# Kernel tuning notes

Hardware: AMD Instinct MI355X
Metric: run time of the kernel (lower is better)

The kernel has to match this reference:

```python
import jax, jax.numpy as jnp
import numpy as np

EPS = 1e-5
GROUPS = 32


def _groupnorm(x, gamma, beta):
    B, C, H, W = x.shape
    xr = x.reshape(B, GROUPS, C // GROUPS, H, W)
    mu = xr.mean(axis=(2, 3, 4), keepdims=True)
    var = xr.var(axis=(2, 3, 4), keepdims=True)
    xn = ((xr - mu) * jax.lax.rsqrt(var + EPS)).reshape(B, C, H, W)
    return xn * gamma[None, :, None, None] + beta[None, :, None, None]


def _conv1x1(x, w, b):
    # x: [B,C,H,W], w: [Cout,Cin], b: [Cout]
    return jnp.einsum('bchw,oc->bohw', x, w) + b[None, :, None, None]


def setup_inputs() -> dict:
    key = jax.random.key(0)
    ks = jax.random.split(key, 11)
    B, C, H, W = 4, 64, 64, 64
    s = 0.05  # weight scale for well-conditioned softmax
    inp = {
        'x': jax.random.normal(ks[0], (B, C, H, W), jnp.float32),
        'gn_gamma': jnp.ones((C,), jnp.float32),
        'gn_beta': jnp.zeros((C,), jnp.float32),
        'wq': jax.random.normal(ks[1], (C, C), jnp.float32) * s,
        'bq': jnp.zeros((C,), jnp.float32),
        'wk': jax.random.normal(ks[2], (C, C), jnp.float32) * s,
        'bk': jnp.zeros((C,), jnp.float32),
        'wv': jax.random.normal(ks[3], (C, C), jnp.float32) * s,
        'bv': jnp.zeros((C,), jnp.float32),
        'wp': jax.random.normal(ks[4], (C, C), jnp.float32) * s,
        'bp': jnp.zeros((C,), jnp.float32),
    }
    return inp


def reference(x, gn_gamma, gn_beta, wq, bq, wk, bk, wv, bv, wp, bp):
    B, C, H, W = x.shape
    h = _groupnorm(x, gn_gamma, gn_beta)
    q = _conv1x1(h, wq, bq)
    k = _conv1x1(h, wk, bk)
    v = _conv1x1(h, wv, bv)
    # scores over all spatial positions: [B,H,W,H,W]
    scale = 1.0 / jnp.sqrt(jnp.asarray(C, x.dtype))
    w = jnp.einsum('bchw,bcHW->bhwHW', q, k) * scale
    w = jax.nn.softmax(w.reshape(B, H, W, H * W), axis=-1).reshape(B, H, W, H, W)
    h = jnp.einsum('bhwHW,bcHW->bchw', w, v)
    h = _conv1x1(h, wp, bp)
    return x + h
```

## Files before the change

kernel.cpp:

```cpp
#include <hip/hip_runtime.h>
#include <stdint.h>

#define Bn 4
#define Cn 64
#define Sn 4096
#define Gn 32

typedef float v4f __attribute__((ext_vector_type(4)));
typedef short v8s __attribute__((ext_vector_type(8)));
typedef short v4s __attribute__((ext_vector_type(4)));

#define MFMA16(a,b,c) __builtin_amdgcn_mfma_f32_16x16x32_bf16((a),(b),(c),0,0,0)

__device__ __forceinline__ float bf2f(uint16_t u){
  union { uint32_t i; float f; } x; x.i = ((uint32_t)u) << 16; return x.f;
}
__device__ __forceinline__ uint16_t f2bf(float f){
  union { float f; uint32_t i; } x; x.f = f;
  uint32_t r = x.i + 0x7fffu + ((x.i >> 16) & 1u);
  return (uint16_t)(r >> 16);
}
__device__ __forceinline__ v8s pack8(float4 a, float4 b){
  v8s r;
  r[0]=(short)f2bf(a.x); r[1]=(short)f2bf(a.y); r[2]=(short)f2bf(a.z); r[3]=(short)f2bf(a.w);
  r[4]=(short)f2bf(b.x); r[5]=(short)f2bf(b.y); r[6]=(short)f2bf(b.z); r[7]=(short)f2bf(b.w);
  return r;
}

__global__ __launch_bounds__(256) void gn_stats(const float* __restrict__ x,
                                                float* __restrict__ stats)
{
  const int tid = threadIdx.x;
  const float* base = x + (size_t)blockIdx.x * 8192;
  float sum = 0.f, sq = 0.f;
  #pragma unroll
  for (int i = 0; i < 8; ++i) {
    float4 v = *(const float4*)(base + ((i << 8) + tid)*4);
    sum += v.x + v.y + v.z + v.w;
    sq  += v.x*v.x + v.y*v.y + v.z*v.z + v.w*v.w;
  }
  #pragma unroll
  for (int off = 1; off < 64; off <<= 1) {
    sum += __shfl_xor(sum, off);
    sq  += __shfl_xor(sq, off);
  }
  __shared__ float red[8];
  const int w = tid >> 6;
  if ((tid & 63) == 0) { red[w] = sum; red[4+w] = sq; }
  __syncthreads();
  if (tid == 0) {
    float s = red[0]+red[1]+red[2]+red[3];
    float q = red[4]+red[5]+red[6]+red[7];
    float mean = s * (1.f/8192.f);
    float var  = q * (1.f/8192.f) - mean*mean;
    stats[blockIdx.x]       = mean;
    stats[128 + blockIdx.x] = rsqrtf(fmaxf(var, 0.f) + 1e-5f);
  }
}

__global__ __launch_bounds__(256) void gn_qkv(
    const float* __restrict__ xg, const float* __restrict__ gamma,
    const float* __restrict__ beta,
    const float* __restrict__ wq, const float* __restrict__ bq,
    const float* __restrict__ wk, const float* __restrict__ bk,
    const float* __restrict__ wv, const float* __restrict__ bv,
    const float* __restrict__ stats,
    uint16_t* __restrict__ Qg, uint16_t* __restrict__ Kg, uint16_t* __restrict__ Vg)
{
  __shared__ uint16_t Hs[16*72];
  const int tid  = threadIdx.x;
  const int w    = tid >> 6;
  const int lane = tid & 63;
  const int l15  = lane & 15;
  const int quad = lane >> 4;
  const int b      = blockIdx.x >> 8;
  const int s_base = (blockIdx.x & 255) << 4;

  {
    const int c = lane;
    const int g = c >> 1;
    const float mean = stats[b*Gn + g];
    const float rstd = stats[128 + b*Gn + g];
    const float ga = gamma[c], be = beta[c];
    float4 v = *(const float4*)(xg + ((size_t)b*Cn + c)*Sn + s_base + (w << 2));
    const int r0 = w << 2;
    Hs[(r0+0)*72 + c] = f2bf((v.x - mean)*rstd*ga + be);
    Hs[(r0+1)*72 + c] = f2bf((v.y - mean)*rstd*ga + be);
    Hs[(r0+2)*72 + c] = f2bf((v.z - mean)*rstd*ga + be);
    Hs[(r0+3)*72 + c] = f2bf((v.w - mean)*rstd*ga + be);
  }
  __syncthreads();

  v8s bh0 = *(const v8s*)(Hs + l15*72 + (quad << 3));
  v8s bh1 = *(const v8s*)(Hs + l15*72 + 32 + (quad << 3));

  #pragma unroll
  for (int t = 0; t < 3; ++t) {
    const int ot   = w*3 + t;
    const int wsel = ot >> 2;
    const int o16  = (ot & 3) << 4;
    const float* Wsel = (wsel == 0) ? wq : (wsel == 1) ? wk : wv;
    const float* Bsel = (wsel == 0) ? bq : (wsel == 1) ? bk : bv;
    const float* Wr = Wsel + (o16 + l15)*64 + (quad << 3);
    v8s a0 = pack8(*(const float4*)(Wr),      *(const float4*)(Wr + 4));
    v8s a1 = pack8(*(const float4*)(Wr + 32), *(const float4*)(Wr + 36));
    v4f d = (v4f){0.f,0.f,0.f,0.f};
    d = MFMA16(a0, bh0, d);
    d = MFMA16(a1, bh1, d);
    const int s = s_base + l15;
    if (wsel <= 1) {
      v4s qv;
      #pragma unroll
      for (int r = 0; r < 4; ++r)
        qv[r] = (short)f2bf(d[r] + Bsel[o16 + (quad << 2) + r]);
      uint16_t* dst = (wsel == 0 ? Qg : Kg) + ((size_t)b*Sn + s)*64 + o16 + (quad << 2);
      *(v4s*)dst = qv;
    } else {
      #pragma unroll
      for (int r = 0; r < 4; ++r) {
        const int o = o16 + (quad << 2) + r;
        Vg[((size_t)b*Cn + o)*Sn + s] = f2bf(d[r] + Bsel[o]);
      }
    }
  }
}

__global__ __launch_bounds__(256) void attn_split(
    const uint16_t* __restrict__ Qg, const uint16_t* __restrict__ Kg,
    const uint16_t* __restrict__ Vg,
    uint16_t* __restrict__ Opart, float* __restrict__ lpart)
{
  __shared__ uint16_t Ks[64*72];
  __shared__ uint16_t Vs[64*72];
  __shared__ uint16_t Ps[4][16*72];

  const int tid  = threadIdx.x;
  const int w    = tid >> 6;
  const int lane = tid & 63;
  const int l15  = lane & 15;
  const int quad = lane >> 4;
  const int bx    = blockIdx.x;
  const int split = bx & 3;
  const int qt    = (bx >> 2) & 63;
  const int b     = bx >> 8;
  const int i_base = qt << 6;
  const int j0     = split << 10;

  const uint16_t* Qb = Qg + ((size_t)b*Sn + i_base)*64;
  const uint16_t* Kb = Kg + (size_t)b*Sn*64;
  const uint16_t* Vb = Vg + (size_t)b*Cn*Sn;

  const int arow = (w << 4) + l15;
  v8s aq0 = *(const v8s*)(Qb + arow*64 + (quad << 3));
  v8s aq1 = *(const v8s*)(Qb + arow*64 + 32 + (quad << 3));

  const int e0 = tid << 3,        r0 = e0 >> 6, c0 = e0 & 63;
  const int e1 = (256 + tid) << 3, r1 = e1 >> 6, c1 = e1 & 63;

  *(v8s*)(Ks + r0*72 + c0) = *(const v8s*)(Kb + j0*64 + e0);
  *(v8s*)(Ks + r1*72 + c1) = *(const v8s*)(Kb + j0*64 + e1);
  *(v8s*)(Vs + r0*72 + c0) = *(const v8s*)(Vb + (size_t)r0*Sn + j0 + c0);
  *(v8s*)(Vs + r1*72 + c1) = *(const v8s*)(Vb + (size_t)r1*Sn + j0 + c1);

  float lsum[4];
  v4f o_acc[4];
  #pragma unroll
  for (int r = 0; r < 4; ++r) lsum[r] = 0.f;
  #pragma unroll
  for (int n = 0; n < 4; ++n) o_acc[n] = (v4f){0.f,0.f,0.f,0.f};

  __syncthreads();

  const float SC = 0.18033688011112042f;

  for (int kt = 0; kt < 16; ++kt) {
    v8s kp0, kp1, vp0, vp1;
    if (kt < 15) {
      const int jb = j0 + ((kt + 1) << 6);
      kp0 = *(const v8s*)(Kb + jb*64 + e0);
      kp1 = *(const v8s*)(Kb + jb*64 + e1);
      vp0 = *(const v8s*)(Vb + (size_t)r0*Sn + jb + c0);
      vp1 = *(const v8s*)(Vb + (size_t)r1*Sn + jb + c1);
    }

    v4f s[4];
    #pragma unroll
    for (int n = 0; n < 4; ++n) {
      const uint16_t* kr = Ks + ((n << 4) + l15)*72;
      v8s b0 = *(const v8s*)(kr + (quad << 3));
      v8s b1 = *(const v8s*)(kr + 32 + (quad << 3));
      v4f t = (v4f){0.f,0.f,0.f,0.f};
      t = MFMA16(aq0, b0, t);
      t = MFMA16(aq1, b1, t);
      s[n] = t;
    }

    uint16_t* Pw = Ps[w];
    #pragma unroll
    for (int n = 0; n < 4; ++n) {
      #pragma unroll
      for (int r = 0; r < 4; ++r) {
        const float pv = __builtin_amdgcn_exp2f(s[n][r]*SC);
        lsum[r] += pv;
        Pw[((quad << 2) + r)*72 + (n << 4) + l15] = f2bf(pv);
      }
    }

    __asm__ volatile("" ::: "memory");

    v8s ap0 = *(const v8s*)(Pw + l15*72 + (quad << 3));
    v8s ap1 = *(const v8s*)(Pw + l15*72 + 32 + (quad << 3));

    #pragma unroll
    for (int n = 0; n < 4; ++n) {
      const uint16_t* vrp = Vs + ((n << 4) + l15)*72;
      v8s b0 = *(const v8s*)(vrp + (quad << 3));
      v8s b1 = *(const v8s*)(vrp + 32 + (quad << 3));
      v4f o = o_acc[n];
      o = MFMA16(ap0, b0, o);
      o = MFMA16(ap1, b1, o);
      o_acc[n] = o;
    }

    __syncthreads();
    if (kt < 15) {
      *(v8s*)(Ks + r0*72 + c0) = kp0;
      *(v8s*)(Ks + r1*72 + c1) = kp1;
      *(v8s*)(Vs + r0*72 + c0) = vp0;
      *(v8s*)(Vs + r1*72 + c1) = vp1;
    }
    __syncthreads();
  }

  #pragma unroll
  for (int r = 0; r < 4; ++r) {
    lsum[r] += __shfl_xor(lsum[r], 1);
    lsum[r] += __shfl_xor(lsum[r], 2);
    lsum[r] += __shfl_xor(lsum[r], 4);
    lsum[r] += __shfl_xor(lsum[r], 8);
  }

  uint16_t* Ob = Opart + (size_t)bx*4096 + (w << 4)*64;
  float*    lp = lpart + bx*64 + (w << 4);
  #pragma unroll
  for (int n = 0; n < 4; ++n)
    #pragma unroll
    for (int r = 0; r < 4; ++r)
      Ob[((quad << 2) + r)*64 + (n << 4) + l15] = f2bf(o_acc[n][r]);
  if (l15 == 0) {
    #pragma unroll
    for (int r = 0; r < 4; ++r) lp[(quad << 2) + r] = lsum[r];
  }
}

__global__ __launch_bounds__(256) void proj_res(
    const uint16_t* __restrict__ Opart, const float* __restrict__ lpart,
    const float* __restrict__ wp, const float* __restrict__ bp,
    const float* __restrict__ xg, float* __restrict__ out)
{
  __shared__ uint16_t As[16*72];
  const int tid  = threadIdx.x;
  const int w    = tid >> 6;
  const int lane = tid & 63;
  const int l15  = lane & 15;
  const int quad = lane >> 4;
  const int b      = blockIdx.x >> 8;
  const int st     = blockIdx.x & 255;
  const int qt     = st >> 2;
  const int sub    = st & 3;
  const int s_base = st << 4;

  const uint16_t* po = Opart + (size_t)((b*64 + qt)*4)*4096 + (sub << 4)*64;
  const float*    pl = lpart + ((b*64 + qt)*4)*64 + (sub << 4);

  {
    const int e = tid << 2, row = tid >> 4, col = (tid & 15) << 2;
    const float linv = 1.f / (pl[row] + pl[64+row] + pl[128+row] + pl[192+row]);
    float acc[4] = {0.f,0.f,0.f,0.f};
    #pragma unroll
    for (int sp = 0; sp < 4; ++sp) {
      v4s o = *(const v4s*)(po + sp*4096 + e);
      #pragma unroll
      for (int j = 0; j < 4; ++j) acc[j] += bf2f((uint16_t)o[j]);
    }
    v4s a;
    #pragma unroll
    for (int j = 0; j < 4; ++j) a[j] = (short)f2bf(acc[j]*linv);
    *(v4s*)(As + row*72 + col) = a;
  }
  __syncthreads();

  v8s ba0 = *(const v8s*)(As + l15*72 + (quad << 3));
  v8s ba1 = *(const v8s*)(As + l15*72 + 32 + (quad << 3));

  const float* Wr = wp + ((w << 4) + l15)*64 + (quad << 3);
  v8s a0 = pack8(*(const float4*)(Wr),      *(const float4*)(Wr + 4));
  v8s a1 = pack8(*(const float4*)(Wr + 32), *(const float4*)(Wr + 36));
  v4f d = (v4f){0.f,0.f,0.f,0.f};
  d = MFMA16(a0, ba0, d);
  d = MFMA16(a1, ba1, d);
  const int s = s_base + l15;
  #pragma unroll
  for (int r = 0; r < 4; ++r) {
    const int o = (w << 4) + (quad << 2) + r;
    const size_t idx = ((size_t)b*Cn + o)*Sn + s;
    out[idx] = d[r] + bp[o] + xg[idx];
  }
}

extern "C" void kernel_launch(void* const* d_in, const int* in_sizes, int n_in,
                              void* d_out, int out_size, void* d_ws, size_t ws_size,
                              hipStream_t stream)
{
  const float* x     = (const float*)d_in[0];
  const float* gamma = (const float*)d_in[1];
  const float* beta  = (const float*)d_in[2];
  const float* wq    = (const float*)d_in[3];
  const float* bq    = (const float*)d_in[4];
  const float* wk    = (const float*)d_in[5];
  const float* bk    = (const float*)d_in[6];
  const float* wv    = (const float*)d_in[7];
  const float* bv    = (const float*)d_in[8];
  const float* wp    = (const float*)d_in[9];
  const float* bp    = (const float*)d_in[10];

  float*    stats = (float*)d_ws;
  uint16_t* Qg    = (uint16_t*)d_ws + 1024;
  uint16_t* Kg    = Qg + (size_t)Bn*Sn*Cn;
  uint16_t* Vg    = Kg + (size_t)Bn*Sn*Cn;
  uint16_t* Opart = Vg + (size_t)Bn*Sn*Cn;
  float*    lpart = (float*)(Opart + (size_t)1024*4096);
  float*    outp  = (float*)d_out;

  gn_stats  <<<128, 256, 0, stream>>>(x, stats);
  gn_qkv    <<<1024, 256, 0, stream>>>(x, gamma, beta, wq, bq, wk, bk, wv, bv,
                                       stats, Qg, Kg, Vg);
  attn_split<<<1024, 256, 0, stream>>>(Qg, Kg, Vg, Opart, lpart);
  proj_res  <<<1024, 256, 0, stream>>>(Opart, lpart, wp, bp, x, outp);
}
```

Measured before the change: 132.1 us.

## Load K/V MFMA operands directly from global memory, drop LDS staging and barriers

The attention kernel no longer stages K and V tiles through shared memory with double-buffered prefetch and two block barriers per iteration. Each wave now reads its MFMA B operands straight from global memory and relies on L2/L1 to serve the reuse across the four waves. The P tile also uses truncating bf16 conversion, and the LDS row pitch changes from 72 to 68 in all kernels. This removes the barrier and LDS traffic but puts repeated global loads on the critical path with no explicit prefetch. It also adds a small rounding bias on P, and the 68-element pitch is not 16-byte aligned for the v8s LDS reads.

```diff
diff --git a/kernel.cpp b/kernel.cpp
--- a/kernel.cpp
+++ b/kernel.cpp
@@ -19,6 +19,10 @@
   union { float f; uint32_t i; } x; x.f = f;
   uint32_t r = x.i + 0x7fffu + ((x.i >> 16) & 1u);
   return (uint16_t)(r >> 16);
+}
+__device__ __forceinline__ uint16_t f2bf_trunc(float f){
+  union { float f; uint32_t i; } x; x.f = f;
+  return (uint16_t)(x.i >> 16);
 }
 __device__ __forceinline__ v8s pack8(float4 a, float4 b){
   v8s r;
@@ -67,7 +71,7 @@
     const float* __restrict__ stats,
     uint16_t* __restrict__ Qg, uint16_t* __restrict__ Kg, uint16_t* __restrict__ Vg)
 {
-  __shared__ uint16_t Hs[16*72];
+  __shared__ uint16_t Hs[16*68];
   const int tid  = threadIdx.x;
   const int w    = tid >> 6;
   const int lane = tid & 63;
@@ -84,15 +88,15 @@
     const float ga = gamma[c], be = beta[c];
     float4 v = *(const float4*)(xg + ((size_t)b*Cn + c)*Sn + s_base + (w << 2));
     const int r0 = w << 2;
-    Hs[(r0+0)*72 + c] = f2bf((v.x - mean)*rstd*ga + be);
-    Hs[(r0+1)*72 + c] = f2bf((v.y - mean)*rstd*ga + be);
-    Hs[(r0+2)*72 + c] = f2bf((v.z - mean)*rstd*ga + be);
-    Hs[(r0+3)*72 + c] = f2bf((v.w - mean)*rstd*ga + be);
+    Hs[(r0+0)*68 + c] = f2bf((v.x - mean)*rstd*ga + be);
+    Hs[(r0+1)*68 + c] = f2bf((v.y - mean)*rstd*ga + be);
+    Hs[(r0+2)*68 + c] = f2bf((v.z - mean)*rstd*ga + be);
+    Hs[(r0+3)*68 + c] = f2bf((v.w - mean)*rstd*ga + be);
   }
   __syncthreads();
 
-  v8s bh0 = *(const v8s*)(Hs + l15*72 + (quad << 3));
-  v8s bh1 = *(const v8s*)(Hs + l15*72 + 32 + (quad << 3));
+  v8s bh0 = *(const v8s*)(Hs + l15*68 + (quad << 3));
+  v8s bh1 = *(const v8s*)(Hs + l15*68 + 32 + (quad << 3));
 
   #pragma unroll
   for (int t = 0; t < 3; ++t) {
@@ -130,9 +134,7 @@
     const uint16_t* __restrict__ Vg,
     uint16_t* __restrict__ Opart, float* __restrict__ lpart)
 {
-  __shared__ uint16_t Ks[64*72];
-  __shared__ uint16_t Vs[64*72];
-  __shared__ uint16_t Ps[4][16*72];
+  __shared__ uint16_t Ps[4][16*68];
 
   const int tid  = threadIdx.x;
   const int w    = tid >> 6;
@@ -154,14 +156,6 @@
   v8s aq0 = *(const v8s*)(Qb + arow*64 + (quad << 3));
   v8s aq1 = *(const v8s*)(Qb + arow*64 + 32 + (quad << 3));
 
-  const int e0 = tid << 3,        r0 = e0 >> 6, c0 = e0 & 63;
-  const int e1 = (256 + tid) << 3, r1 = e1 >> 6, c1 = e1 & 63;
-
-  *(v8s*)(Ks + r0*72 + c0) = *(const v8s*)(Kb + j0*64 + e0);
-  *(v8s*)(Ks + r1*72 + c1) = *(const v8s*)(Kb + j0*64 + e1);
-  *(v8s*)(Vs + r0*72 + c0) = *(const v8s*)(Vb + (size_t)r0*Sn + j0 + c0);
-  *(v8s*)(Vs + r1*72 + c1) = *(const v8s*)(Vb + (size_t)r1*Sn + j0 + c1);
-
   float lsum[4];
   v4f o_acc[4];
   #pragma unroll
@@ -169,24 +163,17 @@
   #pragma unroll
   for (int n = 0; n < 4; ++n) o_acc[n] = (v4f){0.f,0.f,0.f,0.f};
 
-  __syncthreads();
-
   const float SC = 0.18033688011112042f;
-
+  uint16_t* Pw = Ps[w];
+
+  #pragma unroll 2
   for (int kt = 0; kt < 16; ++kt) {
-    v8s kp0, kp1, vp0, vp1;
-    if (kt < 15) {
-      const int jb = j0 + ((kt + 1) << 6);
-      kp0 = *(const v8s*)(Kb + jb*64 + e0);
-      kp1 = *(const v8s*)(Kb + jb*64 + e1);
-      vp0 = *(const v8s*)(Vb + (size_t)r0*Sn + jb + c0);
-      vp1 = *(const v8s*)(Vb + (size_t)r1*Sn + jb + c1);
-    }
+    const int jb = j0 + (kt << 6);
 
     v4f s[4];
     #pragma unroll
     for (int n = 0; n < 4; ++n) {
-      const uint16_t* kr = Ks + ((n << 4) + l15)*72;
+      const uint16_t* kr = Kb + (size_t)(jb + (n << 4) + l15)*64;
       v8s b0 = *(const v8s*)(kr + (quad << 3));
       v8s b1 = *(const v8s*)(kr + 32 + (quad << 3));
       v4f t = (v4f){0.f,0.f,0.f,0.f};
@@ -195,41 +182,33 @@
       s[n] = t;
     }
 
-    uint16_t* Pw = Ps[w];
     #pragma unroll
     for (int n = 0; n < 4; ++n) {
       #pragma unroll
       for (int r = 0; r < 4; ++r) {
         const float pv = __builtin_amdgcn_exp2f(s[n][r]*SC);
         lsum[r] += pv;
-        Pw[((quad << 2) + r)*72 + (n << 4) + l15] = f2bf(pv);
+        Pw[((quad << 2) + r)*68 + (n << 4) + l15] = f2bf_trunc(pv);
       }
     }
 
     __asm__ volatile("" ::: "memory");
 
-    v8s ap0 = *(const v8s*)(Pw + l15*72 + (quad << 3));
-    v8s ap1 = *(const v8s*)(Pw + l15*72 + 32 + (quad << 3));
+    v8s ap0 = *(const v8s*)(Pw + l15*68 + (quad << 3));
+    v8s ap1 = *(const v8s*)(Pw + l15*68 + 32 + (quad << 3));
 
     #pragma unroll
     for (int n = 0; n < 4; ++n) {
-      const uint16_t* vrp = Vs + ((n << 4) + l15)*72;
-      v8s b0 = *(const v8s*)(vrp + (quad << 3));
-      v8s b1 = *(const v8s*)(vrp + 32 + (quad << 3));
+      const uint16_t* vr = Vb + (size_t)((n << 4) + l15)*Sn + jb;
+      v8s b0 = *(const v8s*)(vr + (quad << 3));
+      v8s b1 = *(const v8s*)(vr + 32 + (quad << 3));
       v4f o = o_acc[n];
       o = MFMA16(ap0, b0, o);
       o = MFMA16(ap1, b1, o);
       o_acc[n] = o;
     }
 
-    __syncthreads();
-    if (kt < 15) {
-      *(v8s*)(Ks + r0*72 + c0) = kp0;
-      *(v8s*)(Ks + r1*72 + c1) = kp1;
-      *(v8s*)(Vs + r0*72 + c0) = vp0;
-      *(v8s*)(Vs + r1*72 + c1) = vp1;
-    }
-    __syncthreads();
+    __asm__ volatile("" ::: "memory");
   }
 
   #pragma unroll
@@ -258,7 +237,7 @@
     const float* __restrict__ wp, const float* __restrict__ bp,
     const float* __restrict__ xg, float* __restrict__ out)
 {
-  __shared__ uint16_t As[16*72];
+  __shared__ uint16_t As[16*68];
   const int tid  = threadIdx.x;
   const int w    = tid >> 6;
   const int lane = tid & 63;
@@ -286,12 +265,12 @@
     v4s a;
     #pragma unroll
     for (int j = 0; j < 4; ++j) a[j] = (short)f2bf(acc[j]*linv);
-    *(v4s*)(As + row*72 + col) = a;
+    *(v4s*)(As + row*68 + col) = a;
   }
   __syncthreads();
 
-  v8s ba0 = *(const v8s*)(As + l15*72 + (quad << 3));
-  v8s ba1 = *(const v8s*)(As + l15*72 + 32 + (quad << 3));
+  v8s ba0 = *(const v8s*)(As + l15*68 + (quad << 3));
+  v8s ba1 = *(const v8s*)(As + l15*68 + 32 + (quad << 3));
 
   const float* Wr = wp + ((w << 4) + l15)*64 + (quad << 3);
   v8s a0 = pack8(*(const float4*)(Wr),      *(const float4*)(Wr + 4));
```

After: 211.2 us. +59.9%, slower.
